# Performance work log

Hardware: AMD Instinct MI355X
Metric: run time of the kernel (lower is better)

## Reference

```python
import jax, jax.numpy as jnp
import numpy as np

B, T_CTX, T_PRED = 256, 512, 128
DX, DY, H, L = 7, 1, 256, 2
D_IN = DX + DY  # merged (x, y) feature dim = 8


def _lstm(x, params, h0, c0):
    """Multi-layer LSTM, PyTorch gate order (i, f, g, o).
    x: [B, T, D]; params: list of (W_ih [4H,d], W_hh [4H,H], b_ih, b_hh); h0,c0: [L, B, H].
    Returns (outputs [B,T,H] of top layer, h_T [L,B,H], c_T [L,B,H]).
    """
    def step(carry, x_t):
        h, c = carry
        inp = x_t
        hs, cs = [], []
        for l in range(L):
            Wih, Whh, bih, bhh = params[l]
            gates = inp @ Wih.T + h[l] @ Whh.T + (bih + bhh)  # [B, 4H]
            i, f, g, o = jnp.split(gates, 4, axis=-1)
            c_new = jax.nn.sigmoid(f) * c[l] + jax.nn.sigmoid(i) * jnp.tanh(g)
            h_new = jax.nn.sigmoid(o) * jnp.tanh(c_new)
            hs.append(h_new)
            cs.append(c_new)
            inp = h_new
        return (jnp.stack(hs), jnp.stack(cs)), inp

    (hT, cT), outs = jax.lax.scan(step, (h0, c0), jnp.swapaxes(x, 0, 1))
    return jnp.swapaxes(outs, 0, 1), hT, cT


def setup_inputs() -> dict:
    key = jax.random.key(0)
    ks = jax.random.split(key, 24)
    s = 1.0 / np.sqrt(H)

    def U(k, shape):
        return jax.random.uniform(k, shape, jnp.float32, -s, s)

    inp = {
        "x_context": jax.random.normal(ks[0], (B, T_CTX, DX), jnp.float32),
        "y_context": jax.random.normal(ks[1], (B, T_CTX, DY), jnp.float32),
        "x_target": jax.random.normal(ks[2], (B, T_PRED, DX), jnp.float32),
        "y_target": jax.random.normal(ks[3], (B, T_PRED, DY), jnp.float32),
        "teacher_forcing_prob": 1,
    }
    idx = 4
    for pre in ("enc", "dec"):
        for l in range(L):
            d = D_IN if l == 0 else H
            inp[f"{pre}_Wih{l}"] = U(ks[idx], (4 * H, d)); idx += 1
            inp[f"{pre}_Whh{l}"] = U(ks[idx], (4 * H, H)); idx += 1
            inp[f"{pre}_bih{l}"] = U(ks[idx], (4 * H,)); idx += 1
            inp[f"{pre}_bhh{l}"] = U(ks[idx], (4 * H,)); idx += 1
    inp["fc_W"] = U(ks[idx], (DY, H)); idx += 1
    inp["fc_b"] = U(ks[idx], (DY,))
    return inp


def reference(x_context, y_context, x_target, y_target, teacher_forcing_prob,
              enc_Wih0, enc_Whh0, enc_bih0, enc_bhh0,
              enc_Wih1, enc_Whh1, enc_bih1, enc_bhh1,
              dec_Wih0, dec_Whh0, dec_bih0, dec_bhh0,
              dec_Wih1, dec_Whh1, dec_bih1, dec_bhh1,
              fc_W, fc_b):
    enc_params = [(enc_Wih0, enc_Whh0, enc_bih0, enc_bhh0),
                  (enc_Wih1, enc_Whh1, enc_bih1, enc_bhh1)]
    dec_params = [(dec_Wih0, dec_Whh0, dec_bih0, dec_bhh0),
                  (dec_Wih1, dec_Whh1, dec_bih1, dec_bhh1)]
    b = x_context.shape[0]

    # Encoder over merged context
    merged = jnp.concatenate([x_context, y_context], axis=-1)  # [B, T_CTX, D_IN]
    z = jnp.zeros((L, b, H), merged.dtype)
    _, h, c = _lstm(merged, enc_params, z, z)

    # Decoder: teacher_forcing_prob >= 1 => always teacher-force, so all
    # per-step inputs are known ahead of time and the loop is a single LSTM.
    first = jnp.concatenate([x_context[:, -1], jnp.zeros_like(y_target[:, 0])], axis=-1)[:, None]
    rest = jnp.concatenate([x_target[:, :-1], y_target[:, :-1]], axis=-1)
    dec_in = jnp.concatenate([first, rest], axis=1)  # [B, T_PRED, D_IN]
    outs, _, _ = _lstm(dec_in, dec_params, h, c)  # [B, T_PRED, H]
    return outs @ fc_W.T + fc_b  # [B, T_PRED, DY]
```

## Files before the change

### kernel.cpp

```cpp
#include <hip/hip_runtime.h>
#include <hip/hip_bf16.h>
#include <stdint.h>


namespace {

constexpr int T_CTXC = 512;
constexpr int T_PRED = 128;
constexpr int TTOT   = T_CTXC + T_PRED;
constexpr int K0 = 288;
constexpr int K1 = 512;
constexpr int A0S = 296;
constexpr int A1S = 264;

constexpr size_t OFF_BIAS  = 0;
constexpr size_t OFF_W0E   = 16384;
constexpr size_t OFF_W1E   = OFF_W0E + (size_t)1024 * K0 * 2;
constexpr size_t OFF_W0D   = OFF_W1E + (size_t)1024 * K1 * 2;
constexpr size_t OFF_W1D   = OFF_W0D + (size_t)1024 * K0 * 2;
constexpr size_t OFF_FLAG0 = OFF_W1D + (size_t)1024 * K1 * 2;
constexpr size_t OFF_FLAG1 = OFF_FLAG0 + 1024;
constexpr size_t OFF_H0    = OFF_FLAG1 + 1024;
constexpr size_t OFF_H1    = OFF_H0 + (size_t)2 * 16 * 2048 * 4;
constexpr size_t OFF_OPART = OFF_H1 + (size_t)2 * 16 * 2048 * 4;
constexpr size_t WS_NEEDED = OFF_OPART + (size_t)16 * 256 * 128 * 4;

typedef __attribute__((ext_vector_type(8))) short bf16x8;
typedef __attribute__((ext_vector_type(4))) float f32x4;

__device__ __forceinline__ float fsig(float x) {
    return __builtin_amdgcn_rcpf(1.0f + __expf(-x));
}
__device__ __forceinline__ float ftanh(float x) {
    return 1.0f - 2.0f * __builtin_amdgcn_rcpf(__expf(2.0f * x) + 1.0f);
}

__global__ void prep_kernel(
    const float* __restrict__ eWih0, const float* __restrict__ eWhh0,
    const float* __restrict__ ebih0, const float* __restrict__ ebhh0,
    const float* __restrict__ eWih1, const float* __restrict__ eWhh1,
    const float* __restrict__ ebih1, const float* __restrict__ ebhh1,
    const float* __restrict__ dWih0, const float* __restrict__ dWhh0,
    const float* __restrict__ dbih0, const float* __restrict__ dbhh0,
    const float* __restrict__ dWih1, const float* __restrict__ dWhh1,
    const float* __restrict__ dbih1, const float* __restrict__ dbhh1,
    unsigned char* __restrict__ ws)
{
    __hip_bfloat16* W0e = reinterpret_cast<__hip_bfloat16*>(ws + OFF_W0E);
    __hip_bfloat16* W1e = reinterpret_cast<__hip_bfloat16*>(ws + OFF_W1E);
    __hip_bfloat16* W0d = reinterpret_cast<__hip_bfloat16*>(ws + OFF_W0D);
    __hip_bfloat16* W1d = reinterpret_cast<__hip_bfloat16*>(ws + OFF_W1D);
    float* bias = reinterpret_cast<float*>(ws + OFF_BIAS);
    uint32_t* fl = reinterpret_cast<uint32_t*>(ws + OFF_FLAG0);
    const int stride = gridDim.x * blockDim.x;
    const int tid0 = blockIdx.x * blockDim.x + threadIdx.x;

    for (int idx = tid0; idx < 1024 * K0; idx += stride) {
        int n = idx / K0, k = idx - n * K0;
        float ve, vd;
        if (k < 256)      { ve = eWhh0[n * 256 + k];       vd = dWhh0[n * 256 + k]; }
        else if (k < 264) { ve = eWih0[n * 8 + (k - 256)]; vd = dWih0[n * 8 + (k - 256)]; }
        else              { ve = 0.0f;                     vd = 0.0f; }
        W0e[idx] = __float2bfloat16(ve);
        W0d[idx] = __float2bfloat16(vd);
    }
    for (int idx = tid0; idx < 1024 * K1; idx += stride) {
        int n = idx >> 9, k = idx & 511;
        float ve = (k < 256) ? eWih1[n * 256 + k] : eWhh1[n * 256 + (k - 256)];
        float vd = (k < 256) ? dWih1[n * 256 + k] : dWhh1[n * 256 + (k - 256)];
        W1e[idx] = __float2bfloat16(ve);
        W1d[idx] = __float2bfloat16(vd);
    }
    for (int idx = tid0; idx < 1024; idx += stride) {
        bias[idx]        = ebih0[idx] + ebhh0[idx];
        bias[1024 + idx] = ebih1[idx] + ebhh1[idx];
        bias[2048 + idx] = dbih0[idx] + dbhh0[idx];
        bias[3072 + idx] = dbih1[idx] + dbhh1[idx];
    }
    for (int idx = tid0; idx < 512; idx += stride) fl[idx] = 0;
}

__global__ __launch_bounds__(512, 2) void lstm_kernel(
    const float* __restrict__ xc, const float* __restrict__ yc,
    const float* __restrict__ xt, const float* __restrict__ yt,
    const float* __restrict__ fcW, unsigned char* __restrict__ ws)
{
    __shared__ __align__(16) __hip_bfloat16 A0[16][A0S];
    __shared__ __align__(16) __hip_bfloat16 A1[16][A1S];
    __shared__ float gsm[2][4][16][16];

    const int tid  = threadIdx.x;
    const int lane = tid & 63;
    const int wv   = tid >> 6;
    const int q    = wv & 3;
    const int kh   = wv >> 2;
    const int l15  = lane & 15;
    const int kg   = lane >> 4;
    const int bg   = blockIdx.x >> 4;
    const int ns   = blockIdx.x & 15;

    const float* bias = (const float*)(ws + OFF_BIAS);
    uint32_t* flag0 = (uint32_t*)(ws + OFF_FLAG0) + bg * 16;
    uint32_t* flag1 = (uint32_t*)(ws + OFF_FLAG1) + bg * 16;
    uint32_t* H0_32 = (uint32_t*)(ws + OFF_H0);
    uint32_t* H1_32 = (uint32_t*)(ws + OFF_H1);
    uint64_t* H0_64 = (uint64_t*)(ws + OFF_H0);
    uint64_t* H1_64 = (uint64_t*)(ws + OFF_H1);
    float* opart = (float*)(ws + OFF_OPART);

    const __hip_bfloat16 z16 = __float2bfloat16(0.0f);
    for (int i = tid; i < 16 * A0S; i += 512) (&A0[0][0])[i] = z16;
    for (int i = tid; i < 16 * A1S; i += 512) (&A1[0][0])[i] = z16;
    __syncthreads();
    if (tid < 128) {
        int r = tid >> 3, d = tid & 7, b = bg * 16 + r;
        float v = (d < 7) ? xc[(size_t)(b * T_CTXC) * 7 + d] : yc[b * T_CTXC];
        A0[r][256 + d] = __float2bfloat16(v);
    }

    bf16x8 w0f[5], w1f[8];
    const int wrow = q * 256 + ns * 16 + l15;
    auto load_w = [&](const __hip_bfloat16* W0, const __hip_bfloat16* W1) {
        const __hip_bfloat16* p0 = W0 + (size_t)wrow * K0 + kg * 8;
        const __hip_bfloat16* p1 = W1 + (size_t)wrow * K1 + kg * 8;
        if (kh == 0) {
            #pragma unroll
            for (int f = 0; f < 4; ++f) w0f[f] = *reinterpret_cast<const bf16x8*>(p0 + f * 32);
            #pragma unroll
            for (int f = 0; f < 8; ++f) w1f[f] = *reinterpret_cast<const bf16x8*>(p1 + f * 32);
        } else {
            #pragma unroll
            for (int f = 0; f < 5; ++f) w0f[f] = *reinterpret_cast<const bf16x8*>(p0 + (4 + f) * 32);
            #pragma unroll
            for (int f = 0; f < 8; ++f) w1f[f] = *reinterpret_cast<const bf16x8*>(p1 + (8 + f) * 32);
        }
    };
    load_w((const __hip_bfloat16*)(ws + OFF_W0E), (const __hip_bfloat16*)(ws + OFF_W1E));

    const int crow = tid >> 4;
    const int ccol = tid & 15;
    const int gcol = ns * 16 + ccol;
    float c0v = 0.f, c1v = 0.f;
    float b0r[4] = {0,0,0,0}, b1r[4] = {0,0,0,0}, fcw_r = 0.f;
    if (tid < 256) {
        #pragma unroll
        for (int qq = 0; qq < 4; ++qq) {
            b0r[qq] = bias[qq * 256 + gcol];
            b1r[qq] = bias[1024 + qq * 256 + gcol];
        }
        fcw_r = fcW[gcol];
    }
    __syncthreads();

    for (int t = 0; t < TTOT; ++t) {
        if (t == T_CTXC) {
            load_w((const __hip_bfloat16*)(ws + OFF_W0D), (const __hip_bfloat16*)(ws + OFF_W1D));
            if (tid < 256) {
                #pragma unroll
                for (int qq = 0; qq < 4; ++qq) {
                    b0r[qq] = bias[2048 + qq * 256 + gcol];
                    b1r[qq] = bias[3072 + qq * 256 + gcol];
                }
            }
        }
        const int par = t & 1;
        const size_t hbase32 = (size_t)(par * 16 + bg) * 2048;
        const size_t hbase64 = (size_t)(par * 16 + bg) * 1024;

        {
            f32x4 acc = {0.f, 0.f, 0.f, 0.f};
            if (kh == 0) {
                #pragma unroll
                for (int f = 0; f < 4; ++f) {
                    bf16x8 a = *reinterpret_cast<const bf16x8*>(&A0[l15][f * 32 + kg * 8]);
                    acc = __builtin_amdgcn_mfma_f32_16x16x32_bf16(a, w0f[f], acc, 0, 0, 0);
                }
            } else {
                #pragma unroll
                for (int f = 0; f < 5; ++f) {
                    bf16x8 a = *reinterpret_cast<const bf16x8*>(&A0[l15][(4 + f) * 32 + kg * 8]);
                    acc = __builtin_amdgcn_mfma_f32_16x16x32_bf16(a, w0f[f], acc, 0, 0, 0);
                }
            }
            #pragma unroll
            for (int r = 0; r < 4; ++r) gsm[kh][q][kg * 4 + r][l15] = acc[r];
        }
        __syncthreads();

        if (tid < 256) {
            float gi = gsm[0][0][crow][ccol] + gsm[1][0][crow][ccol] + b0r[0];
            float gf = gsm[0][1][crow][ccol] + gsm[1][1][crow][ccol] + b0r[1];
            float gg = gsm[0][2][crow][ccol] + gsm[1][2][crow][ccol] + b0r[2];
            float go = gsm[0][3][crow][ccol] + gsm[1][3][crow][ccol] + b0r[3];
            c0v = fsig(gf) * c0v + fsig(gi) * ftanh(gg);
            float h = fsig(go) * ftanh(c0v);
            __hip_bfloat16 hb = __float2bfloat16(h);
            unsigned short hbits; __builtin_memcpy(&hbits, &hb, 2);
            uint32_t hu = hbits;
            uint32_t pr = (uint32_t)__shfl_xor((int)hu, 1);
            if ((ccol & 1) == 0) {
                uint32_t v = (hu & 0xffffu) | (pr << 16);
                __hip_atomic_store(&H0_32[hbase32 + crow * 128 + (gcol >> 1)], v,
                                   __ATOMIC_RELAXED, __HIP_MEMORY_SCOPE_AGENT);
            }
        }
        asm volatile("s_waitcnt vmcnt(0)" ::: "memory");
        __syncthreads();
        if (tid == 0)
            __hip_atomic_store(&flag0[ns], (uint32_t)(t + 1),
                               __ATOMIC_RELAXED, __HIP_MEMORY_SCOPE_AGENT);

        {
            int tn = t + 1;
            if (tid < 128 && tn < TTOT) {
                int r = tid >> 3, d = tid & 7, b = bg * 16 + r;
                float v;
                if (tn < T_CTXC)       v = (d < 7) ? xc[(size_t)(b * T_CTXC + tn) * 7 + d] : yc[b * T_CTXC + tn];
                else if (tn == T_CTXC) v = (d < 7) ? xc[(size_t)(b * T_CTXC + T_CTXC - 1) * 7 + d] : 0.0f;
                else { int u = tn - T_CTXC - 1;
                       v = (d < 7) ? xt[(size_t)(b * T_PRED + u) * 7 + d] : yt[b * T_PRED + u]; }
                A0[r][256 + d] = __float2bfloat16(v);
            }
        }
        if (tid < 16) {
            while (__hip_atomic_load(&flag0[tid], __ATOMIC_RELAXED, __HIP_MEMORY_SCOPE_AGENT)
                   < (uint32_t)(t + 1))
                __builtin_amdgcn_s_sleep(1);
        }
        __syncthreads();
        {
            uint64_t d0 = __hip_atomic_load(&H0_64[hbase64 + tid * 2 + 0],
                                            __ATOMIC_RELAXED, __HIP_MEMORY_SCOPE_AGENT);
            uint64_t d1 = __hip_atomic_load(&H0_64[hbase64 + tid * 2 + 1],
                                            __ATOMIC_RELAXED, __HIP_MEMORY_SCOPE_AGENT);
            int row = tid >> 5, c0i = (tid & 31) * 8;
            uint4 v = make_uint4((uint32_t)d0, (uint32_t)(d0 >> 32),
                                 (uint32_t)d1, (uint32_t)(d1 >> 32));
            *reinterpret_cast<uint4*>(&A0[row][c0i]) = v;
        }
        __syncthreads();

        {
            f32x4 acc = {0.f, 0.f, 0.f, 0.f};
            if (kh == 0) {
                #pragma unroll
                for (int f = 0; f < 8; ++f) {
                    bf16x8 a = *reinterpret_cast<const bf16x8*>(&A0[l15][f * 32 + kg * 8]);
                    acc = __builtin_amdgcn_mfma_f32_16x16x32_bf16(a, w1f[f], acc, 0, 0, 0);
                }
            } else {
                #pragma unroll
                for (int f = 0; f < 8; ++f) {
                    bf16x8 a = *reinterpret_cast<const bf16x8*>(&A1[l15][f * 32 + kg * 8]);
                    acc = __builtin_amdgcn_mfma_f32_16x16x32_bf16(a, w1f[f], acc, 0, 0, 0);
                }
            }
            #pragma unroll
            for (int r = 0; r < 4; ++r) gsm[kh][q][kg * 4 + r][l15] = acc[r];
        }
        __syncthreads();

        if (tid < 256) {
            float gi = gsm[0][0][crow][ccol] + gsm[1][0][crow][ccol] + b1r[0];
            float gf = gsm[0][1][crow][ccol] + gsm[1][1][crow][ccol] + b1r[1];
            float gg = gsm[0][2][crow][ccol] + gsm[1][2][crow][ccol] + b1r[2];
            float go = gsm[0][3][crow][ccol] + gsm[1][3][crow][ccol] + b1r[3];
            c1v = fsig(gf) * c1v + fsig(gi) * ftanh(gg);
            float h = fsig(go) * ftanh(c1v);
            __hip_bfloat16 hb = __float2bfloat16(h);
            unsigned short hbits; __builtin_memcpy(&hbits, &hb, 2);
            uint32_t hu = hbits;
            uint32_t pr = (uint32_t)__shfl_xor((int)hu, 1);
            if ((ccol & 1) == 0) {
                uint32_t v = (hu & 0xffffu) | (pr << 16);
                __hip_atomic_store(&H1_32[hbase32 + crow * 128 + (gcol >> 1)], v,
                                   __ATOMIC_RELAXED, __HIP_MEMORY_SCOPE_AGENT);
            }
            if (t >= T_CTXC) {
                float p = h * fcw_r;
                p += __shfl_xor(p, 1);
                p += __shfl_xor(p, 2);
                p += __shfl_xor(p, 4);
                p += __shfl_xor(p, 8);
                if (ccol == 0)
                    opart[(size_t)ns * (256 * T_PRED)
                          + (size_t)(bg * 16 + crow) * T_PRED + (t - T_CTXC)] = p;
            }
        }
        asm volatile("s_waitcnt vmcnt(0)" ::: "memory");
        __syncthreads();
        if (tid == 0)
            __hip_atomic_store(&flag1[ns], (uint32_t)(t + 1),
                               __ATOMIC_RELAXED, __HIP_MEMORY_SCOPE_AGENT);

        if (tid < 16) {
            while (__hip_atomic_load(&flag1[tid], __ATOMIC_RELAXED, __HIP_MEMORY_SCOPE_AGENT)
                   < (uint32_t)(t + 1))
                __builtin_amdgcn_s_sleep(1);
        }
        __syncthreads();
        {
            uint64_t d0 = __hip_atomic_load(&H1_64[hbase64 + tid * 2 + 0],
                                            __ATOMIC_RELAXED, __HIP_MEMORY_SCOPE_AGENT);
            uint64_t d1 = __hip_atomic_load(&H1_64[hbase64 + tid * 2 + 1],
                                            __ATOMIC_RELAXED, __HIP_MEMORY_SCOPE_AGENT);
            int row = tid >> 5, c0i = (tid & 31) * 8;
            uint4 v = make_uint4((uint32_t)d0, (uint32_t)(d0 >> 32),
                                 (uint32_t)d1, (uint32_t)(d1 >> 32));
            *reinterpret_cast<uint4*>(&A1[row][c0i]) = v;
        }
        __syncthreads();
    }
}

__global__ void out_kernel(const float* __restrict__ fcb,
                           const unsigned char* __restrict__ ws,
                           float* __restrict__ out)
{
    int i = blockIdx.x * blockDim.x + threadIdx.x;
    if (i >= 256 * T_PRED) return;
    const float* op = (const float*)(ws + OFF_OPART);
    float s = fcb[0];
    #pragma unroll
    for (int j = 0; j < 16; ++j) s += op[(size_t)j * (256 * T_PRED) + i];
    out[i] = s;
}

}

extern "C" void kernel_launch(void* const* d_in, const int* in_sizes, int n_in,
                              void* d_out, int out_size, void* d_ws, size_t ws_size,
                              hipStream_t stream)
{
    if (ws_size < WS_NEEDED) return;

    const float* xc    = (const float*)d_in[0];
    const float* yc    = (const float*)d_in[1];
    const float* xt    = (const float*)d_in[2];
    const float* yt    = (const float*)d_in[3];
    const float* eWih0 = (const float*)d_in[5];
    const float* eWhh0 = (const float*)d_in[6];
    const float* ebih0 = (const float*)d_in[7];
    const float* ebhh0 = (const float*)d_in[8];
    const float* eWih1 = (const float*)d_in[9];
    const float* eWhh1 = (const float*)d_in[10];
    const float* ebih1 = (const float*)d_in[11];
    const float* ebhh1 = (const float*)d_in[12];
    const float* dWih0 = (const float*)d_in[13];
    const float* dWhh0 = (const float*)d_in[14];
    const float* dbih0 = (const float*)d_in[15];
    const float* dbhh0 = (const float*)d_in[16];
    const float* dWih1 = (const float*)d_in[17];
    const float* dWhh1 = (const float*)d_in[18];
    const float* dbih1 = (const float*)d_in[19];
    const float* dbhh1 = (const float*)d_in[20];
    const float* fcW   = (const float*)d_in[21];
    const float* fcb   = (const float*)d_in[22];

    unsigned char* wsb = (unsigned char*)d_ws;

    hipLaunchKernelGGL(prep_kernel, dim3(1024), dim3(256), 0, stream,
                       eWih0, eWhh0, ebih0, ebhh0, eWih1, eWhh1, ebih1, ebhh1,
                       dWih0, dWhh0, dbih0, dbhh0, dWih1, dWhh1, dbih1, dbhh1, wsb);

    void* kargs[] = { (void*)&xc, (void*)&yc, (void*)&xt, (void*)&yt,
                      (void*)&fcW, (void*)&wsb };
    hipError_t ce = hipLaunchCooperativeKernel(lstm_kernel, dim3(256), dim3(512),
                                               kargs, 0, stream);
    if (ce != hipSuccess) {
        hipLaunchKernelGGL(lstm_kernel, dim3(256), dim3(512), 0, stream,
                           xc, yc, xt, yt, fcW, wsb);
    }

    hipLaunchKernelGGL(out_kernel, dim3((256 * T_PRED + 255) / 256), dim3(256), 0, stream,
                       fcb, (const unsigned char*)wsb, (float*)d_out);
}
```

Before: 3.194 ms.

## Wavefront-skew LSTM layers to halve per-step grid syncs and fuse output reduction

Restructures the persistent LSTM loop so that layer 0 at step t+1 is computed in the same phase as layer 1 at step t. Both hidden states are published together, which cuts the cross-block flag barriers per timestep from two to one. The separate output-reduction kernel is removed and replaced with atomicAdd into a zeroed output buffer, which adds a memset launch and makes the float summation order nondeterministic. A prologue runs layer 0's first step, and the encoder-to-decoder weight switch is staggered between the two layers.

```diff
diff --git a/kernel.cpp b/kernel.cpp
--- a/kernel.cpp
+++ b/kernel.cpp
@@ -9,21 +9,17 @@
 constexpr int T_PRED = 128;
 constexpr int TTOT   = T_CTXC + T_PRED;
 constexpr int K0 = 288;
-constexpr int K1 = 512;
-constexpr int A0S = 296;
-constexpr int A1S = 264;
-
-constexpr size_t OFF_BIAS  = 0;
-constexpr size_t OFF_W0E   = 16384;
-constexpr size_t OFF_W1E   = OFF_W0E + (size_t)1024 * K0 * 2;
-constexpr size_t OFF_W0D   = OFF_W1E + (size_t)1024 * K1 * 2;
-constexpr size_t OFF_W1D   = OFF_W0D + (size_t)1024 * K0 * 2;
-constexpr size_t OFF_FLAG0 = OFF_W1D + (size_t)1024 * K1 * 2;
-constexpr size_t OFF_FLAG1 = OFF_FLAG0 + 1024;
-constexpr size_t OFF_H0    = OFF_FLAG1 + 1024;
-constexpr size_t OFF_H1    = OFF_H0 + (size_t)2 * 16 * 2048 * 4;
-constexpr size_t OFF_OPART = OFF_H1 + (size_t)2 * 16 * 2048 * 4;
-constexpr size_t WS_NEEDED = OFF_OPART + (size_t)16 * 256 * 128 * 4;
+constexpr int HAS = 296;
+constexpr int HBS = 264;
+
+constexpr size_t OFF_BIAS = 0;
+constexpr size_t OFF_W0E  = 16384;
+constexpr size_t OFF_W1E  = OFF_W0E + (size_t)1024 * K0 * 2;
+constexpr size_t OFF_W0D  = OFF_W1E + (size_t)1024 * 512 * 2;
+constexpr size_t OFF_W1D  = OFF_W0D + (size_t)1024 * K0 * 2;
+constexpr size_t OFF_FLAG = OFF_W1D + (size_t)1024 * 512 * 2;
+constexpr size_t OFF_H    = OFF_FLAG + 1024;
+constexpr size_t WS_NEEDED = OFF_H + (size_t)2 * 16 * 32 * 128 * 4;
 
 typedef __attribute__((ext_vector_type(8))) short bf16x8;
 typedef __attribute__((ext_vector_type(4))) float f32x4;
@@ -51,7 +47,7 @@
     __hip_bfloat16* W0d = reinterpret_cast<__hip_bfloat16*>(ws + OFF_W0D);
     __hip_bfloat16* W1d = reinterpret_cast<__hip_bfloat16*>(ws + OFF_W1D);
     float* bias = reinterpret_cast<float*>(ws + OFF_BIAS);
-    uint32_t* fl = reinterpret_cast<uint32_t*>(ws + OFF_FLAG0);
+    uint32_t* fl = reinterpret_cast<uint32_t*>(ws + OFF_FLAG);
     const int stride = gridDim.x * blockDim.x;
     const int tid0 = blockIdx.x * blockDim.x + threadIdx.x;
 
@@ -64,7 +60,7 @@
         W0e[idx] = __float2bfloat16(ve);
         W0d[idx] = __float2bfloat16(vd);
     }
-    for (int idx = tid0; idx < 1024 * K1; idx += stride) {
+    for (int idx = tid0; idx < 1024 * 512; idx += stride) {
         int n = idx >> 9, k = idx & 511;
         float ve = (k < 256) ? eWih1[n * 256 + k] : eWhh1[n * 256 + (k - 256)];
         float vd = (k < 256) ? dWih1[n * 256 + k] : dWhh1[n * 256 + (k - 256)];
@@ -77,17 +73,19 @@
         bias[2048 + idx] = dbih0[idx] + dbhh0[idx];
         bias[3072 + idx] = dbih1[idx] + dbhh1[idx];
     }
-    for (int idx = tid0; idx < 512; idx += stride) fl[idx] = 0;
+    for (int idx = tid0; idx < 256; idx += stride) fl[idx] = 0;
 }
 
 __global__ __launch_bounds__(512, 2) void lstm_kernel(
     const float* __restrict__ xc, const float* __restrict__ yc,
     const float* __restrict__ xt, const float* __restrict__ yt,
-    const float* __restrict__ fcW, unsigned char* __restrict__ ws)
+    const float* __restrict__ fcW, const float* __restrict__ fcb,
+    unsigned char* __restrict__ ws, float* __restrict__ out)
 {
-    __shared__ __align__(16) __hip_bfloat16 A0[16][A0S];
-    __shared__ __align__(16) __hip_bfloat16 A1[16][A1S];
-    __shared__ float gsm[2][4][16][16];
+    __shared__ __align__(16) __hip_bfloat16 HA[16][HAS];
+    __shared__ __align__(16) __hip_bfloat16 HB[16][HBS];
+    __shared__ float gsm0[2][4][16][16];
+    __shared__ float gsm1[2][4][16][16];
 
     const int tid  = threadIdx.x;
     const int lane = tid & 63;
@@ -100,48 +98,45 @@
     const int ns   = blockIdx.x & 15;
 
     const float* bias = (const float*)(ws + OFF_BIAS);
-    uint32_t* flag0 = (uint32_t*)(ws + OFF_FLAG0) + bg * 16;
-    uint32_t* flag1 = (uint32_t*)(ws + OFF_FLAG1) + bg * 16;
-    uint32_t* H0_32 = (uint32_t*)(ws + OFF_H0);
-    uint32_t* H1_32 = (uint32_t*)(ws + OFF_H1);
-    uint64_t* H0_64 = (uint64_t*)(ws + OFF_H0);
-    uint64_t* H1_64 = (uint64_t*)(ws + OFF_H1);
-    float* opart = (float*)(ws + OFF_OPART);
+    uint32_t* flag = (uint32_t*)(ws + OFF_FLAG) + bg * 16;
+    uint32_t* H32  = (uint32_t*)(ws + OFF_H);
+    uint64_t* H64  = (uint64_t*)(ws + OFF_H);
 
     const __hip_bfloat16 z16 = __float2bfloat16(0.0f);
-    for (int i = tid; i < 16 * A0S; i += 512) (&A0[0][0])[i] = z16;
-    for (int i = tid; i < 16 * A1S; i += 512) (&A1[0][0])[i] = z16;
+    for (int i = tid; i < 16 * HAS; i += 512) (&HA[0][0])[i] = z16;
     __syncthreads();
     if (tid < 128) {
         int r = tid >> 3, d = tid & 7, b = bg * 16 + r;
         float v = (d < 7) ? xc[(size_t)(b * T_CTXC) * 7 + d] : yc[b * T_CTXC];
-        A0[r][256 + d] = __float2bfloat16(v);
+        HA[r][256 + d] = __float2bfloat16(v);
     }
 
     bf16x8 w0f[5], w1f[8];
     const int wrow = q * 256 + ns * 16 + l15;
-    auto load_w = [&](const __hip_bfloat16* W0, const __hip_bfloat16* W1) {
+    auto load_w0 = [&](const __hip_bfloat16* W0) {
         const __hip_bfloat16* p0 = W0 + (size_t)wrow * K0 + kg * 8;
-        const __hip_bfloat16* p1 = W1 + (size_t)wrow * K1 + kg * 8;
         if (kh == 0) {
             #pragma unroll
             for (int f = 0; f < 4; ++f) w0f[f] = *reinterpret_cast<const bf16x8*>(p0 + f * 32);
-            #pragma unroll
-            for (int f = 0; f < 8; ++f) w1f[f] = *reinterpret_cast<const bf16x8*>(p1 + f * 32);
         } else {
             #pragma unroll
             for (int f = 0; f < 5; ++f) w0f[f] = *reinterpret_cast<const bf16x8*>(p0 + (4 + f) * 32);
-            #pragma unroll
-            for (int f = 0; f < 8; ++f) w1f[f] = *reinterpret_cast<const bf16x8*>(p1 + (8 + f) * 32);
         }
     };
-    load_w((const __hip_bfloat16*)(ws + OFF_W0E), (const __hip_bfloat16*)(ws + OFF_W1E));
+    auto load_w1 = [&](const __hip_bfloat16* W1) {
+        const __hip_bfloat16* p1 = W1 + (size_t)wrow * 512 + kg * 8;
+        #pragma unroll
+        for (int f = 0; f < 8; ++f)
+            w1f[f] = *reinterpret_cast<const bf16x8*>(p1 + (kh * 8 + f) * 32);
+    };
+    load_w0((const __hip_bfloat16*)(ws + OFF_W0E));
+    load_w1((const __hip_bfloat16*)(ws + OFF_W1E));
 
     const int crow = tid >> 4;
     const int ccol = tid & 15;
     const int gcol = ns * 16 + ccol;
     float c0v = 0.f, c1v = 0.f;
-    float b0r[4] = {0,0,0,0}, b1r[4] = {0,0,0,0}, fcw_r = 0.f;
+    float b0r[4] = {0,0,0,0}, b1r[4] = {0,0,0,0}, fcw_r = 0.f, fcb_v = 0.f;
     if (tid < 256) {
         #pragma unroll
         for (int qq = 0; qq < 4; ++qq) {
@@ -149,69 +144,99 @@
             b1r[qq] = bias[1024 + qq * 256 + gcol];
         }
         fcw_r = fcW[gcol];
+        if (ns == 0) fcb_v = fcb[0];
     }
     __syncthreads();
 
-    for (int t = 0; t < TTOT; ++t) {
-        if (t == T_CTXC) {
-            load_w((const __hip_bfloat16*)(ws + OFF_W0D), (const __hip_bfloat16*)(ws + OFF_W1D));
+    {
+        f32x4 acc = {0.f, 0.f, 0.f, 0.f};
+        if (kh == 0) {
+            #pragma unroll
+            for (int f = 0; f < 4; ++f) {
+                bf16x8 a = *reinterpret_cast<const bf16x8*>(&HA[l15][f * 32 + kg * 8]);
+                acc = __builtin_amdgcn_mfma_f32_16x16x32_bf16(a, w0f[f], acc, 0, 0, 0);
+            }
+        } else {
+            #pragma unroll
+            for (int f = 0; f < 5; ++f) {
+                bf16x8 a = *reinterpret_cast<const bf16x8*>(&HA[l15][(4 + f) * 32 + kg * 8]);
+                acc = __builtin_amdgcn_mfma_f32_16x16x32_bf16(a, w0f[f], acc, 0, 0, 0);
+            }
+        }
+        #pragma unroll
+        for (int r = 0; r < 4; ++r) gsm0[kh][q][kg * 4 + r][l15] = acc[r];
+    }
+    __syncthreads();
+    if (tid < 256) {
+        float gi = gsm0[0][0][crow][ccol] + gsm0[1][0][crow][ccol] + b0r[0];
+        float gf = gsm0[0][1][crow][ccol] + gsm0[1][1][crow][ccol] + b0r[1];
+        float gg = gsm0[0][2][crow][ccol] + gsm0[1][2][crow][ccol] + b0r[2];
+        float go = gsm0[0][3][crow][ccol] + gsm0[1][3][crow][ccol] + b0r[3];
+        c0v = fsig(gf) * c0v + fsig(gi) * ftanh(gg);
+        float h = fsig(go) * ftanh(c0v);
+        __hip_bfloat16 hb = __float2bfloat16(h);
+        unsigned short hbits; __builtin_memcpy(&hbits, &hb, 2);
+        uint32_t hu = hbits;
+        uint32_t pr = (uint32_t)__shfl_xor((int)hu, 1);
+        if ((ccol & 1) == 0) {
+            uint32_t v = (hu & 0xffffu) | (pr << 16);
+            size_t base = ((size_t)bg * 32 + crow) * 128 + (gcol >> 1);
+            __hip_atomic_store(&H32[base], v, __ATOMIC_RELAXED, __HIP_MEMORY_SCOPE_AGENT);
+            __hip_atomic_store(&H32[base + 16 * 128], 0u,
+                               __ATOMIC_RELAXED, __HIP_MEMORY_SCOPE_AGENT);
+        }
+    }
+    asm volatile("s_waitcnt vmcnt(0)" ::: "memory");
+    __syncthreads();
+    if (tid == 0)
+        __hip_atomic_store(&flag[ns], 1u, __ATOMIC_RELAXED, __HIP_MEMORY_SCOPE_AGENT);
+
+    for (int i = 0; i < TTOT; ++i) {
+        const bool last = (i == TTOT - 1);
+        if (i == T_CTXC - 1) {
+            load_w0((const __hip_bfloat16*)(ws + OFF_W0D));
             if (tid < 256) {
                 #pragma unroll
-                for (int qq = 0; qq < 4; ++qq) {
-                    b0r[qq] = bias[2048 + qq * 256 + gcol];
-                    b1r[qq] = bias[3072 + qq * 256 + gcol];
-                }
-            }
-        }
-        const int par = t & 1;
-        const size_t hbase32 = (size_t)(par * 16 + bg) * 2048;
-        const size_t hbase64 = (size_t)(par * 16 + bg) * 1024;
+                for (int qq = 0; qq < 4; ++qq) b0r[qq] = bias[2048 + qq * 256 + gcol];
+            }
+        }
+        if (i == T_CTXC) {
+            load_w1((const __hip_bfloat16*)(ws + OFF_W1D));
+            if (tid < 256) {
+                #pragma unroll
+                for (int qq = 0; qq < 4; ++qq) b1r[qq] = bias[3072 + qq * 256 + gcol];
+            }
+        }
+        const int par = i & 1;
+
+        if (tid < 16) {
+            while (__hip_atomic_load(&flag[tid], __ATOMIC_RELAXED, __HIP_MEMORY_SCOPE_AGENT)
+                   < (uint32_t)(i + 1))
+                __builtin_amdgcn_s_sleep(1);
+        }
+        __syncthreads();
 
         {
-            f32x4 acc = {0.f, 0.f, 0.f, 0.f};
-            if (kh == 0) {
-                #pragma unroll
-                for (int f = 0; f < 4; ++f) {
-                    bf16x8 a = *reinterpret_cast<const bf16x8*>(&A0[l15][f * 32 + kg * 8]);
-                    acc = __builtin_amdgcn_mfma_f32_16x16x32_bf16(a, w0f[f], acc, 0, 0, 0);
-                }
+            int row = tid >> 4, cb = tid & 15;
+            const uint64_t* src = H64 + ((size_t)(par * 16 + bg) * 32 + row) * 64 + cb * 4;
+            uint64_t d0 = __hip_atomic_load(&src[0], __ATOMIC_RELAXED, __HIP_MEMORY_SCOPE_AGENT);
+            uint64_t d1 = __hip_atomic_load(&src[1], __ATOMIC_RELAXED, __HIP_MEMORY_SCOPE_AGENT);
+            uint64_t d2 = __hip_atomic_load(&src[2], __ATOMIC_RELAXED, __HIP_MEMORY_SCOPE_AGENT);
+            uint64_t d3 = __hip_atomic_load(&src[3], __ATOMIC_RELAXED, __HIP_MEMORY_SCOPE_AGENT);
+            uint4 v0 = make_uint4((uint32_t)d0, (uint32_t)(d0 >> 32),
+                                  (uint32_t)d1, (uint32_t)(d1 >> 32));
+            uint4 v1 = make_uint4((uint32_t)d2, (uint32_t)(d2 >> 32),
+                                  (uint32_t)d3, (uint32_t)(d3 >> 32));
+            if (row < 16) {
+                *reinterpret_cast<uint4*>(&HA[row][cb * 16]) = v0;
+                *reinterpret_cast<uint4*>(&HA[row][cb * 16 + 8]) = v1;
             } else {
-                #pragma unroll
-                for (int f = 0; f < 5; ++f) {
-                    bf16x8 a = *reinterpret_cast<const bf16x8*>(&A0[l15][(4 + f) * 32 + kg * 8]);
-                    acc = __builtin_amdgcn_mfma_f32_16x16x32_bf16(a, w0f[f], acc, 0, 0, 0);
-                }
-            }
-            #pragma unroll
-            for (int r = 0; r < 4; ++r) gsm[kh][q][kg * 4 + r][l15] = acc[r];
-        }
-        __syncthreads();
-
-        if (tid < 256) {
-            float gi = gsm[0][0][crow][ccol] + gsm[1][0][crow][ccol] + b0r[0];
-            float gf = gsm[0][1][crow][ccol] + gsm[1][1][crow][ccol] + b0r[1];
-            float gg = gsm[0][2][crow][ccol] + gsm[1][2][crow][ccol] + b0r[2];
-            float go = gsm[0][3][crow][ccol] + gsm[1][3][crow][ccol] + b0r[3];
-            c0v = fsig(gf) * c0v + fsig(gi) * ftanh(gg);
-            float h = fsig(go) * ftanh(c0v);
-            __hip_bfloat16 hb = __float2bfloat16(h);
-            unsigned short hbits; __builtin_memcpy(&hbits, &hb, 2);
-            uint32_t hu = hbits;
-            uint32_t pr = (uint32_t)__shfl_xor((int)hu, 1);
-            if ((ccol & 1) == 0) {
-                uint32_t v = (hu & 0xffffu) | (pr << 16);
-                __hip_atomic_store(&H0_32[hbase32 + crow * 128 + (gcol >> 1)], v,
-                                   __ATOMIC_RELAXED, __HIP_MEMORY_SCOPE_AGENT);
-            }
-        }
-        asm volatile("s_waitcnt vmcnt(0)" ::: "memory");
-        __syncthreads();
-        if (tid == 0)
-            __hip_atomic_store(&flag0[ns], (uint32_t)(t + 1),
-                               __ATOMIC_RELAXED, __HIP_MEMORY_SCOPE_AGENT);
-
+                *reinterpret_cast<uint4*>(&HB[row - 16][cb * 16]) = v0;
+                *reinterpret_cast<uint4*>(&HB[row - 16][cb * 16 + 8]) = v1;
+            }
+        }
         {
-            int tn = t + 1;
+            int tn = i + 1;
             if (tid < 128 && tn < TTOT) {
                 int r = tid >> 3, d = tid & 7, b = bg * 16 + r;
                 float v;
@@ -219,24 +244,8 @@
                 else if (tn == T_CTXC) v = (d < 7) ? xc[(size_t)(b * T_CTXC + T_CTXC - 1) * 7 + d] : 0.0f;
                 else { int u = tn - T_CTXC - 1;
                        v = (d < 7) ? xt[(size_t)(b * T_PRED + u) * 7 + d] : yt[b * T_PRED + u]; }
-                A0[r][256 + d] = __float2bfloat16(v);
-            }
-        }
-        if (tid < 16) {
-            while (__hip_atomic_load(&flag0[tid], __ATOMIC_RELAXED, __HIP_MEMORY_SCOPE_AGENT)
-                   < (uint32_t)(t + 1))
-                __builtin_amdgcn_s_sleep(1);
-        }
-        __syncthreads();
-        {
-            uint64_t d0 = __hip_atomic_load(&H0_64[hbase64 + tid * 2 + 0],
-                                            __ATOMIC_RELAXED, __HIP_MEMORY_SCOPE_AGENT);
-            uint64_t d1 = __hip_atomic_load(&H0_64[hbase64 + tid * 2 + 1],
-                                            __ATOMIC_RELAXED, __HIP_MEMORY_SCOPE_AGENT);
-            int row = tid >> 5, c0i = (tid & 31) * 8;
-            uint4 v = make_uint4((uint32_t)d0, (uint32_t)(d0 >> 32),
-                                 (uint32_t)d1, (uint32_t)(d1 >> 32));
-            *reinterpret_cast<uint4*>(&A0[row][c0i]) = v;
+                HA[r][256 + d] = __float2bfloat16(v);
+            }
         }
         __syncthreads();
 
@@ -245,85 +254,97 @@
             if (kh == 0) {
                 #pragma unroll
                 for (int f = 0; f < 8; ++f) {
-                    bf16x8 a = *reinterpret_cast<const bf16x8*>(&A0[l15][f * 32 + kg * 8]);
+                    bf16x8 a = *reinterpret_cast<const bf16x8*>(&HA[l15][f * 32 + kg * 8]);
                     acc = __builtin_amdgcn_mfma_f32_16x16x32_bf16(a, w1f[f], acc, 0, 0, 0);
                 }
             } else {
                 #pragma unroll
                 for (int f = 0; f < 8; ++f) {
-                    bf16x8 a = *reinterpret_cast<const bf16x8*>(&A1[l15][f * 32 + kg * 8]);
+                    bf16x8 a = *reinterpret_cast<const bf16x8*>(&HB[l15][f * 32 + kg * 8]);
                     acc = __builtin_amdgcn_mfma_f32_16x16x32_bf16(a, w1f[f], acc, 0, 0, 0);
                 }
             }
             #pragma unroll
-            for (int r = 0; r < 4; ++r) gsm[kh][q][kg * 4 + r][l15] = acc[r];
+            for (int r = 0; r < 4; ++r) gsm1[kh][q][kg * 4 + r][l15] = acc[r];
+        }
+        if (!last) {
+            f32x4 acc = {0.f, 0.f, 0.f, 0.f};
+            if (kh == 0) {
+                #pragma unroll
+                for (int f = 0; f < 4; ++f) {
+                    bf16x8 a = *reinterpret_cast<const bf16x8*>(&HA[l15][f * 32 + kg * 8]);
+                    acc = __builtin_amdgcn_mfma_f32_16x16x32_bf16(a, w0f[f], acc, 0, 0, 0);
+                }
+            } else {
+                #pragma unroll
+                for (int f = 0; f < 5; ++f) {
+                    bf16x8 a = *reinterpret_cast<const bf16x8*>(&HA[l15][(4 + f) * 32 + kg * 8]);
+                    acc = __builtin_amdgcn_mfma_f32_16x16x32_bf16(a, w0f[f], acc, 0, 0, 0);
+                }
+            }
+            #pragma unroll
+            for (int r = 0; r < 4; ++r) gsm0[kh][q][kg * 4 + r][l15] = acc[r];
         }
         __syncthreads();
 
         if (tid < 256) {
-            float gi = gsm[0][0][crow][ccol] + gsm[1][0][crow][ccol] + b1r[0];
-            float gf = gsm[0][1][crow][ccol] + gsm[1][1][crow][ccol] + b1r[1];
-            float gg = gsm[0][2][crow][ccol] + gsm[1][2][crow][ccol] + b1r[2];
-            float go = gsm[0][3][crow][ccol] + gsm[1][3][crow][ccol] + b1r[3];
-            c1v = fsig(gf) * c1v + fsig(gi) * ftanh(gg);
-            float h = fsig(go) * ftanh(c1v);
-            __hip_bfloat16 hb = __float2bfloat16(h);
-            unsigned short hbits; __builtin_memcpy(&hbits, &hb, 2);
-            uint32_t hu = hbits;
-            uint32_t pr = (uint32_t)__shfl_xor((int)hu, 1);
-            if ((ccol & 1) == 0) {
-                uint32_t v = (hu & 0xffffu) | (pr << 16);
-                __hip_atomic_store(&H1_32[hbase32 + crow * 128 + (gcol >> 1)], v,
+            const int par2 = (i + 1) & 1;
+            const size_t base = ((size_t)(par2 * 16 + bg) * 32 + crow) * 128 + (gcol >> 1);
+            {
+                float gi = gsm1[0][0][crow][ccol] + gsm1[1][0][crow][ccol] + b1r[0];
+                float gf = gsm1[0][1][crow][ccol] + gsm1[1][1][crow][ccol] + b1r[1];
+                float gg = gsm1[0][2][crow][ccol] + gsm1[1][2][crow][ccol] + b1r[2];
+                float go = gsm1[0][3][crow][ccol] + gsm1[1][3][crow][ccol] + b1r[3];
+                c1v = fsig(gf) * c1v + fsig(gi) * ftanh(gg);
+                float h = fsig(go) * ftanh(c1v);
+                if (!last) {
+                    __hip_bfloat16 hb = __float2bfloat16(h);
+                    unsigned short hbits; __builtin_memcpy(&hbits, &hb, 2);
+                    uint32_t hu = hbits;
+                    uint32_t pr = (uint32_t)__shfl_xor((int)hu, 1);
+                    if ((ccol & 1) == 0) {
+                        uint32_t v = (hu & 0xffffu) | (pr << 16);
+                        __hip_atomic_store(&H32[base + 16 * 128], v,
+                                           __ATOMIC_RELAXED, __HIP_MEMORY_SCOPE_AGENT);
+                    }
+                }
+                if (i >= T_CTXC) {
+                    float p = h * fcw_r;
+                    p += __shfl_xor(p, 1);
+                    p += __shfl_xor(p, 2);
+                    p += __shfl_xor(p, 4);
+                    p += __shfl_xor(p, 8);
+                    if (ccol == 0)
+                        atomicAdd(&out[(size_t)(bg * 16 + crow) * T_PRED + (i - T_CTXC)],
+                                  p + fcb_v);
+                }
+            }
+            if (!last) {
+                float gi = gsm0[0][0][crow][ccol] + gsm0[1][0][crow][ccol] + b0r[0];
+                float gf = gsm0[0][1][crow][ccol] + gsm0[1][1][crow][ccol] + b0r[1];
+                float gg = gsm0[0][2][crow][ccol] + gsm0[1][2][crow][ccol] + b0r[2];
+                float go = gsm0[0][3][crow][ccol] + gsm0[1][3][crow][ccol] + b0r[3];
+                c0v = fsig(gf) * c0v + fsig(gi) * ftanh(gg);
+                float h = fsig(go) * ftanh(c0v);
+                __hip_bfloat16 hb = __float2bfloat16(h);
+                unsigned short hbits; __builtin_memcpy(&hbits, &hb, 2);
+                uint32_t hu = hbits;
+                uint32_t pr = (uint32_t)__shfl_xor((int)hu, 1);
+                if ((ccol & 1) == 0) {
+                    uint32_t v = (hu & 0xffffu) | (pr << 16);
+                    __hip_atomic_store(&H32[base], v,
+                                       __ATOMIC_RELAXED, __HIP_MEMORY_SCOPE_AGENT);
+                }
+            }
+        }
+        if (!last) {
+            asm volatile("s_waitcnt vmcnt(0)" ::: "memory");
+            __syncthreads();
+            if (tid == 0)
+                __hip_atomic_store(&flag[ns], (uint32_t)(i + 2),
                                    __ATOMIC_RELAXED, __HIP_MEMORY_SCOPE_AGENT);
-            }
-            if (t >= T_CTXC) {
-                float p = h * fcw_r;
-                p += __shfl_xor(p, 1);
-                p += __shfl_xor(p, 2);
-                p += __shfl_xor(p, 4);
-                p += __shfl_xor(p, 8);
-                if (ccol == 0)
-                    opart[(size_t)ns * (256 * T_PRED)
-                          + (size_t)(bg * 16 + crow) * T_PRED + (t - T_CTXC)] = p;
-            }
-        }
-        asm volatile("s_waitcnt vmcnt(0)" ::: "memory");
-        __syncthreads();
-        if (tid == 0)
-            __hip_atomic_store(&flag1[ns], (uint32_t)(t + 1),
-                               __ATOMIC_RELAXED, __HIP_MEMORY_SCOPE_AGENT);
-
-        if (tid < 16) {
-            while (__hip_atomic_load(&flag1[tid], __ATOMIC_RELAXED, __HIP_MEMORY_SCOPE_AGENT)
-                   < (uint32_t)(t + 1))
-                __builtin_amdgcn_s_sleep(1);
-        }
-        __syncthreads();
-        {
-            uint64_t d0 = __hip_atomic_load(&H1_64[hbase64 + tid * 2 + 0],
-                                            __ATOMIC_RELAXED, __HIP_MEMORY_SCOPE_AGENT);
-            uint64_t d1 = __hip_atomic_load(&H1_64[hbase64 + tid * 2 + 1],
-                                            __ATOMIC_RELAXED, __HIP_MEMORY_SCOPE_AGENT);
-            int row = tid >> 5, c0i = (tid & 31) * 8;
-            uint4 v = make_uint4((uint32_t)d0, (uint32_t)(d0 >> 32),
-                                 (uint32_t)d1, (uint32_t)(d1 >> 32));
-            *reinterpret_cast<uint4*>(&A1[row][c0i]) = v;
-        }
-        __syncthreads();
-    }
-}
-
-__global__ void out_kernel(const float* __restrict__ fcb,
-                           const unsigned char* __restrict__ ws,
-                           float* __restrict__ out)
-{
-    int i = blockIdx.x * blockDim.x + threadIdx.x;
-    if (i >= 256 * T_PRED) return;
-    const float* op = (const float*)(ws + OFF_OPART);
-    float s = fcb[0];
-    #pragma unroll
-    for (int j = 0; j < 16; ++j) s += op[(size_t)j * (256 * T_PRED) + i];
-    out[i] = s;
+        }
+    }
 }
 
 }
@@ -358,20 +379,20 @@
     const float* fcb   = (const float*)d_in[22];
 
     unsigned char* wsb = (unsigned char*)d_ws;
+    float* outp = (float*)d_out;
 
     hipLaunchKernelGGL(prep_kernel, dim3(1024), dim3(256), 0, stream,
                        eWih0, eWhh0, ebih0, ebhh0, eWih1, eWhh1, ebih1, ebhh1,
                        dWih0, dWhh0, dbih0, dbhh0, dWih1, dWhh1, dbih1, dbhh1, wsb);
 
+    hipMemsetAsync(d_out, 0, (size_t)out_size * sizeof(float), stream);
+
     void* kargs[] = { (void*)&xc, (void*)&yc, (void*)&xt, (void*)&yt,
-                      (void*)&fcW, (void*)&wsb };
+                      (void*)&fcW, (void*)&fcb, (void*)&wsb, (void*)&outp };
     hipError_t ce = hipLaunchCooperativeKernel(lstm_kernel, dim3(256), dim3(512),
                                                kargs, 0, stream);
     if (ce != hipSuccess) {
         hipLaunchKernelGGL(lstm_kernel, dim3(256), dim3(512), 0, stream,
-                           xc, yc, xt, yt, fcW, wsb);
-    }
-
-    hipLaunchKernelGGL(out_kernel, dim3((256 * T_PRED + 255) / 256), dim3(256), 0, stream,
-                       fcb, (const unsigned char*)wsb, (float*)d_out);
-}
+                           xc, yc, xt, yt, fcW, fcb, wsb, outp);
+    }
+}
```

Result: faster. 2.938 ms (-8.0%).
